# Performance work log

Hardware: AMD Instinct MI355X
Metric: run time of the kernel (lower is better)

Reference implementation:

```python
import jax, jax.numpy as jnp
import numpy as np

N = 100000        # unique nodes in batch (node_num)
IN_DIM = 256
OUT_DIM = 128
E_RAND = 1_600_000  # random graph edges (avg degree 16)
B = N             # batch nodes (all nodes, each gets a self-loop edge)
SLOPE = 0.1       # leaky_relu slope_ratio


def setup_inputs() -> dict:
    key = jax.random.key(0)
    k1, k2, k3, k4, k5, k6 = jax.random.split(key, 6)
    x = jax.random.normal(k1, (N, IN_DIM), dtype=jnp.float32)
    # small weight scale keeps exp(leaky_relu(.)) in a sane range, like kaiming on unit-ish inputs
    W = jax.random.normal(k2, (OUT_DIM, IN_DIM), dtype=jnp.float32) * 0.05
    b = jax.random.normal(k3, (OUT_DIM,), dtype=jnp.float32) * 0.05
    a = jax.random.normal(k4, (2 * OUT_DIM, 1), dtype=jnp.float32) * 0.05
    src = jax.random.randint(k5, (E_RAND,), 0, N, dtype=jnp.int32)
    dst = jax.random.randint(k6, (E_RAND,), 0, N, dtype=jnp.int32)
    batch_idx = jnp.arange(B, dtype=jnp.int32)
    # append self-loop edges for every batch node (original vstacks original_node_edge)
    edges = jnp.stack([jnp.concatenate([src, batch_idx]),
                       jnp.concatenate([dst, batch_idx])], axis=1)  # [E_TOT, 2]
    return {"x": x, "W": W, "b": b, "a": a, "edges": edges, "batch_idx": batch_idx}


def reference(x, W, b, a, edges, batch_idx):
    # new_embeddings = Linear(in_dim -> out_dim)
    emb = x @ W.T + b  # [N, out_dim]
    # concat(h_src, h_dst) @ a  ==  h_src @ a[:d] + h_dst @ a[d:]
    a1 = a[:OUT_DIM, 0]
    a2 = a[OUT_DIM:, 0]
    s_src = emb @ a1  # [N]
    s_dst = emb @ a2  # [N]
    src, dst = edges[:, 0], edges[:, 1]
    logits = s_src[src] + s_dst[dst]                                 # [E]
    score = jnp.exp(jax.nn.leaky_relu(logits, negative_slope=SLOPE))  # [E]
    # sparse row-sum and aggregation fused as segment reductions over src
    row_sum = jax.ops.segment_sum(score, src, num_segments=N)        # [N]
    msgs = score[:, None] * emb[dst]                                 # [E, out_dim]
    results = jax.ops.segment_sum(msgs, src, num_segments=N)         # [N, out_dim]
    # nodes with no outgoing edges have row_sum==0; they are never gathered below
    safe_rs = jnp.where(row_sum > 0, row_sum, 1.0)
    out = results / safe_rs[:, None]
    return out[batch_idx]
```

## Files before the change

kernel.cpp:

```cpp
#include <hip/hip_runtime.h>
#include <hip/hip_fp16.h>

#define IN_DIM 256
#define OUT_DIM 128
#define SLOPE 0.1f

typedef __attribute__((ext_vector_type(8))) short short8;
typedef __attribute__((ext_vector_type(4))) float f32x4;

__device__ __forceinline__ unsigned bf16_rne(float f) {
    unsigned u = __float_as_uint(f);
    return (u + 0x7FFFu + ((u >> 16) & 1u)) >> 16;
}

__global__ __launch_bounds__(256) void wsplit_kernel(
    const float* __restrict__ W, short* __restrict__ Whi, short* __restrict__ Wlo)
{
    const int i = blockIdx.x * 256 + threadIdx.x;
    const float v = W[i];
    const unsigned hb = bf16_rne(v);
    const float hf = __uint_as_float(hb << 16);
    Whi[i] = (short)hb;
    Wlo[i] = (short)bf16_rne(v - hf);
}

__global__ __launch_bounds__(256) void gemm_emb_kernel(
    const float* __restrict__ x, const short* __restrict__ Whi_g,
    const short* __restrict__ Wlo_g, const float* __restrict__ bias,
    const float* __restrict__ a, __half* __restrict__ emb_h,
    float* __restrict__ s1, float* __restrict__ s2, int N)
{
    __shared__ short lds[12288];
    short* Ahi = lds;
    short* Alo = lds + 2048;
    short* Bhi = lds + 4096;
    short* Blo = lds + 8192;

    const int tid = threadIdx.x;
    const int l   = tid & 63;
    const int w   = tid >> 6;
    const int gm0 = blockIdx.x * 64;

    const int arow = tid >> 2;
    const int akc  = tid & 3;
    const int gmA  = gm0 + arow;
    const bool av_ok = (gmA < N);
    const int brow = tid >> 1;
    const int bkc0 = (tid & 1) * 2;

    f32x4 acc[8];
    #pragma unroll
    for (int j = 0; j < 8; ++j) acc[j] = (f32x4)0.f;

    float bias_v[8], av1[8], av2[8];
    #pragma unroll
    for (int nf = 0; nf < 8; ++nf) {
        const int col = nf * 16 + (l & 15);
        bias_v[nf] = bias[col];
        av1[nf]    = a[col];
        av2[nf]    = a[OUT_DIM + col];
    }

    for (int ks = 0; ks < 8; ++ks) {
        const int k0 = ks * 32;
        {
            float v[8];
            if (av_ok) {
                const float4 p0 = *(const float4*)&x[(size_t)gmA * IN_DIM + k0 + akc * 8];
                const float4 p1 = *(const float4*)&x[(size_t)gmA * IN_DIM + k0 + akc * 8 + 4];
                v[0]=p0.x; v[1]=p0.y; v[2]=p0.z; v[3]=p0.w;
                v[4]=p1.x; v[5]=p1.y; v[6]=p1.z; v[7]=p1.w;
            } else {
                #pragma unroll
                for (int j = 0; j < 8; ++j) v[j] = 0.f;
            }
            short8 h8, l8;
            #pragma unroll
            for (int j = 0; j < 8; ++j) {
                unsigned hb = bf16_rne(v[j]);
                float hf = __uint_as_float(hb << 16);
                h8[j] = (short)hb;
                l8[j] = (short)bf16_rne(v[j] - hf);
            }
            *(short8*)&Ahi[akc * 512 + arow * 8] = h8;
            *(short8*)&Alo[akc * 512 + arow * 8] = l8;
        }
        #pragma unroll
        for (int q = 0; q < 2; ++q) {
            const int kc = bkc0 + q;
            const short8 h8 = *(const short8*)&Whi_g[brow * IN_DIM + k0 + kc * 8];
            const short8 l8 = *(const short8*)&Wlo_g[brow * IN_DIM + k0 + kc * 8];
            *(short8*)&Bhi[kc * 1024 + brow * 8] = h8;
            *(short8*)&Blo[kc * 1024 + brow * 8] = l8;
        }
        __syncthreads();

        const int arow_f = w * 16 + (l & 15);
        const int aoff   = (l >> 4) * 512 + arow_f * 8;
        const short8 ah = *(const short8*)&Ahi[aoff];
        const short8 al = *(const short8*)&Alo[aoff];
        #pragma unroll
        for (int nf = 0; nf < 8; ++nf) {
            const int col = nf * 16 + (l & 15);
            const int boff = (l >> 4) * 1024 + col * 8;
            const short8 bh = *(const short8*)&Bhi[boff];
            const short8 bl = *(const short8*)&Blo[boff];
            acc[nf] = __builtin_amdgcn_mfma_f32_16x16x32_bf16(ah, bh, acc[nf], 0, 0, 0);
            acc[nf] = __builtin_amdgcn_mfma_f32_16x16x32_bf16(al, bh, acc[nf], 0, 0, 0);
            acc[nf] = __builtin_amdgcn_mfma_f32_16x16x32_bf16(ah, bl, acc[nf], 0, 0, 0);
        }
        __syncthreads();
    }

    __half* hl = (__half*)lds;
    #pragma unroll
    for (int r = 0; r < 4; ++r) {
        const int lrow = w * 16 + (l >> 4) * 4 + r;
        float p1 = 0.f, p2 = 0.f;
        #pragma unroll
        for (int nf = 0; nf < 8; ++nf) {
            const float e = acc[nf][r] + bias_v[nf];
            p1 += e * av1[nf];
            p2 += e * av2[nf];
            hl[lrow * 144 + nf * 16 + (l & 15)] = __float2half(e);
        }
        p1 += __shfl_xor(p1, 1); p1 += __shfl_xor(p1, 2);
        p1 += __shfl_xor(p1, 4); p1 += __shfl_xor(p1, 8);
        p2 += __shfl_xor(p2, 1); p2 += __shfl_xor(p2, 2);
        p2 += __shfl_xor(p2, 4); p2 += __shfl_xor(p2, 8);
        const int gm = gm0 + lrow;
        if ((l & 15) == 0 && gm < N) { s1[gm] = p1; s2[gm] = p2; }
    }
    __syncthreads();
    #pragma unroll
    for (int i = 0; i < 4; ++i) {
        const int idx = i * 256 + tid;
        const int row = idx >> 4, seg = idx & 15;
        if (gm0 + row < N) {
            const uint4 u = *(const uint4*)&hl[row * 144 + seg * 8];
            ((uint4*)emb_h)[(size_t)(gm0 + row) * 16 + seg] = u;
        }
    }
}

__global__ __launch_bounds__(256) void rank_kernel(
    const int* __restrict__ edges, int* __restrict__ deg,
    int* __restrict__ rank, int E)
{
    const int e0 = (blockIdx.x * 256 + threadIdx.x) * 4;
    if (e0 + 3 < E) {
        const int4 ea = ((const int4*)edges)[(e0 >> 1) + 0];
        const int4 eb = ((const int4*)edges)[(e0 >> 1) + 1];
        const int r0 = atomicAdd(&deg[ea.x], 1);
        const int r1 = atomicAdd(&deg[ea.z], 1);
        const int r2 = atomicAdd(&deg[eb.x], 1);
        const int r3 = atomicAdd(&deg[eb.z], 1);
        ((int4*)rank)[e0 >> 2] = make_int4(r0, r1, r2, r3);
    } else if (e0 < E) {
        for (int e = e0; e < E; ++e) {
            const int2 ed = ((const int2*)edges)[e];
            rank[e] = atomicAdd(&deg[ed.x], 1);
        }
    }
}

__global__ __launch_bounds__(256) void scan1_kernel(
    const int* __restrict__ deg, int* __restrict__ off,
    int* __restrict__ bsum, int N)
{
    __shared__ int lds[256];
    const int t = threadIdx.x;
    const int base = blockIdx.x * 1024 + t * 4;
    int v[4];
    int ts = 0;
    #pragma unroll
    for (int j = 0; j < 4; ++j) {
        v[j] = (base + j < N) ? deg[base + j] : 0;
        ts += v[j];
    }
    lds[t] = ts;
    __syncthreads();
    for (int d = 1; d < 256; d <<= 1) {
        int xv = (t >= d) ? lds[t - d] : 0;
        __syncthreads();
        lds[t] += xv;
        __syncthreads();
    }
    int run = lds[t] - ts;
    #pragma unroll
    for (int j = 0; j < 4; ++j) {
        if (base + j < N) off[base + j] = run;
        run += v[j];
    }
    if (t == 255) bsum[blockIdx.x] = lds[255];
}

__global__ __launch_bounds__(256) void scan2_kernel(int* __restrict__ bsum, int nb)
{
    __shared__ int lds[256];
    const int t = threadIdx.x;
    const int v = (t < nb) ? bsum[t] : 0;
    lds[t] = v;
    __syncthreads();
    for (int d = 1; d < 256; d <<= 1) {
        int xv = (t >= d) ? lds[t - d] : 0;
        __syncthreads();
        lds[t] += xv;
        __syncthreads();
    }
    if (t < nb) bsum[t] = lds[t] - v;
}

__global__ __launch_bounds__(256) void scan3_kernel(
    int* __restrict__ off, const int* __restrict__ bsum,
    const int* __restrict__ bidx, int* __restrict__ flag, int N, int E)
{
    const int i = blockIdx.x * 256 + threadIdx.x;
    if (i < N) {
        off[i] += bsum[i >> 10];
        if (bidx[i] != i) atomicOr(flag, 1);
    }
    if (i == 0) off[N] = E;
}

__global__ __launch_bounds__(256) void fill_kernel(
    const int* __restrict__ edges, const int* __restrict__ off,
    const int* __restrict__ rank, int* __restrict__ csr, int E)
{
    const int e0 = (blockIdx.x * 256 + threadIdx.x) * 4;
    if (e0 + 3 < E) {
        const int4 ea = ((const int4*)edges)[(e0 >> 1) + 0];
        const int4 eb = ((const int4*)edges)[(e0 >> 1) + 1];
        const int4 rk = ((const int4*)rank)[e0 >> 2];
        csr[off[ea.x] + rk.x] = ea.y;
        csr[off[ea.z] + rk.y] = ea.w;
        csr[off[eb.x] + rk.z] = eb.y;
        csr[off[eb.z] + rk.w] = eb.w;
    } else if (e0 < E) {
        for (int e = e0; e < E; ++e) {
            const int2 ed = ((const int2*)edges)[e];
            csr[off[ed.x] + rank[e]] = ed.y;
        }
    }
}

__global__ __launch_bounds__(256) void agg_kernel(
    const int* __restrict__ off, const int* __restrict__ csr,
    const float* __restrict__ s1, const float* __restrict__ s2,
    const __half* __restrict__ emb_h, const int* __restrict__ flag,
    float* __restrict__ results, float* __restrict__ out, int N)
{
    const int wid  = (int)((blockIdx.x * 256u + threadIdx.x) >> 6);
    const int lane = threadIdx.x & 63;
    if (wid >= N) return;
    const int eg = lane >> 4;
    const int cl = lane & 15;
    const int beg = off[wid];
    const int end = off[wid + 1];
    const float s1n = s1[wid];

    const float4* __restrict__ embrow = (const float4*)emb_h;

    float av[8];
    #pragma unroll
    for (int k = 0; k < 8; ++k) av[k] = 0.f;
    float rs = 0.f;

    for (int base = beg; base < end; base += 16) {
        int dq[4];
        #pragma unroll
        for (int q = 0; q < 4; ++q) {
            const int idx = base + q * 4 + eg;
            dq[q] = (idx < end) ? csr[idx] : -1;
        }
        float scq[4];
        #pragma unroll
        for (int q = 0; q < 4; ++q) {
            if (dq[q] >= 0) {
                const float ll = s1n + s2[dq[q]];
                scq[q] = __expf(ll > 0.f ? ll : SLOPE * ll);
            } else {
                scq[q] = 0.f;
                dq[q]  = 0;
            }
        }
        float4 vq[4];
        #pragma unroll
        for (int q = 0; q < 4; ++q)
            vq[q] = embrow[(size_t)dq[q] * 16 + cl];
        #pragma unroll
        for (int q = 0; q < 4; ++q) {
            rs += scq[q];
            const __half2* hp = reinterpret_cast<const __half2*>(&vq[q]);
            #pragma unroll
            for (int k = 0; k < 4; ++k) {
                const float2 f = __half22float2(hp[k]);
                av[2 * k]     += scq[q] * f.x;
                av[2 * k + 1] += scq[q] * f.y;
            }
        }
    }

    #pragma unroll
    for (int k = 0; k < 8; ++k) {
        av[k] += __shfl_xor(av[k], 16);
        av[k] += __shfl_xor(av[k], 32);
    }
    rs += __shfl_xor(rs, 16);
    rs += __shfl_xor(rs, 32);

    const float inv = 1.f / (rs > 0.f ? rs : 1.f);
    if (eg == 0) {
        float* dbuf = (*flag == 0) ? out : results;
        float4* rp = (float4*)&dbuf[(size_t)wid * 128 + cl * 8];
        rp[0] = make_float4(av[0] * inv, av[1] * inv, av[2] * inv, av[3] * inv);
        rp[1] = make_float4(av[4] * inv, av[5] * inv, av[6] * inv, av[7] * inv);
    }
}

__global__ __launch_bounds__(256) void gather_kernel(
    const float* __restrict__ results, const int* __restrict__ bidx,
    const int* __restrict__ flag, float* __restrict__ out, int N)
{
    if (*flag == 0) return;
    const unsigned i = blockIdx.x * 256u + threadIdx.x;
    if (i >= (unsigned)N * 32u) return;
    const unsigned n = i >> 5, c = i & 31;
    ((float4*)out)[i] = ((const float4*)results)[(size_t)bidx[n] * 32 + c];
}

extern "C" void kernel_launch(void* const* d_in, const int* in_sizes, int n_in,
                              void* d_out, int out_size, void* d_ws, size_t ws_size,
                              hipStream_t stream) {
    const float* x     = (const float*)d_in[0];
    const float* W     = (const float*)d_in[1];
    const float* b     = (const float*)d_in[2];
    const float* a     = (const float*)d_in[3];
    const int*   edges = (const int*)d_in[4];
    const int*   bidx  = (const int*)d_in[5];

    const int N = in_sizes[5];
    const int E = in_sizes[4] / 2;

    float*  results = (float*)d_ws;
    __half* emb_h   = (__half*)(results + (size_t)N * OUT_DIM);
    int*    rank    = (int*)(emb_h + (size_t)N * OUT_DIM);
    int*    csr     = rank + E;
    float*  s1      = (float*)(csr + E);
    float*  s2      = s1 + N;
    int*    deg     = (int*)(s2 + N);
    int*    flag    = deg + N;
    int*    off     = flag + 1;
    int*    bsum    = off + N + 1;
    short*  Whi     = (short*)(bsum + 256);
    short*  Wlo     = Whi + OUT_DIM * IN_DIM;

    hipMemsetAsync(deg, 0, (size_t)(N + 1) * sizeof(int), stream);

    wsplit_kernel<<<(OUT_DIM * IN_DIM) / 256, 256, 0, stream>>>(W, Whi, Wlo);

    dim3 gGemm((N + 63) / 64);
    gemm_emb_kernel<<<gGemm, 256, 0, stream>>>(x, Whi, Wlo, b, a, emb_h, s1, s2, N);

    const int gE4 = (E / 4 + 255) / 256 + 1;
    rank_kernel<<<gE4, 256, 0, stream>>>(edges, deg, rank, E);

    const int nb = (N + 1023) / 1024;
    scan1_kernel<<<nb, 256, 0, stream>>>(deg, off, bsum, N);
    scan2_kernel<<<1, 256, 0, stream>>>(bsum, nb);
    scan3_kernel<<<(N + 255) / 256, 256, 0, stream>>>(off, bsum, bidx, flag, N, E);

    fill_kernel<<<gE4, 256, 0, stream>>>(edges, off, rank, csr, E);

    const unsigned aggThreads = (unsigned)N * 64u;
    agg_kernel<<<(aggThreads + 255u) / 256u, 256, 0, stream>>>(
        off, csr, s1, s2, emb_h, flag, results, (float*)d_out, N);

    const unsigned gatherThreads = (unsigned)N * 32u;
    gather_kernel<<<(gatherThreads + 255u) / 256u, 256, 0, stream>>>(
        results, bidx, flag, (float*)d_out, N);
}
```

Before: 229.7 us.

## Stage edge scores in LDS per wave and fold block-sum scan into scan3

The aggregation kernel now computes each edge's destination index and attention score once per lane (64 edges per tile), stashes them in a per-wave LDS slot, and then has the four 16-lane groups read them back to issue up to 8 embedding-row loads at a time. This removes the redundant s2 gathers and exp evaluations that each lane group previously did, and raises memory-level parallelism per iteration. Separately, the single-block scan2 kernel is removed: scan3 now sums the preceding block sums itself with a shared-memory reduction, saving one launch at the cost of redundant small reductions in every block.

```diff
diff --git a/kernel.cpp b/kernel.cpp
--- a/kernel.cpp
+++ b/kernel.cpp
@@ -195,29 +195,26 @@
     if (t == 255) bsum[blockIdx.x] = lds[255];
 }
 
-__global__ __launch_bounds__(256) void scan2_kernel(int* __restrict__ bsum, int nb)
-{
-    __shared__ int lds[256];
-    const int t = threadIdx.x;
-    const int v = (t < nb) ? bsum[t] : 0;
-    lds[t] = v;
-    __syncthreads();
-    for (int d = 1; d < 256; d <<= 1) {
-        int xv = (t >= d) ? lds[t - d] : 0;
-        __syncthreads();
-        lds[t] += xv;
-        __syncthreads();
-    }
-    if (t < nb) bsum[t] = lds[t] - v;
-}
-
 __global__ __launch_bounds__(256) void scan3_kernel(
     int* __restrict__ off, const int* __restrict__ bsum,
     const int* __restrict__ bidx, int* __restrict__ flag, int N, int E)
 {
-    const int i = blockIdx.x * 256 + threadIdx.x;
+    __shared__ int red[256];
+    const int t = threadIdx.x;
+    const int chunk = (int)(blockIdx.x >> 2);
+    int s = 0;
+    for (int j = t; j < chunk; j += 256) s += bsum[j];
+    red[t] = s;
+    __syncthreads();
+    #pragma unroll
+    for (int d = 128; d > 0; d >>= 1) {
+        if (t < d) red[t] += red[t + d];
+        __syncthreads();
+    }
+    const int pref = red[0];
+    const int i = blockIdx.x * 256 + t;
     if (i < N) {
-        off[i] += bsum[i >> 10];
+        off[i] += pref;
         if (bidx[i] != i) atomicOr(flag, 1);
     }
     if (i == 0) off[N] = E;
@@ -250,8 +247,11 @@
     const __half* __restrict__ emb_h, const int* __restrict__ flag,
     float* __restrict__ results, float* __restrict__ out, int N)
 {
+    __shared__ int2 sl[4][64];
+
     const int wid  = (int)((blockIdx.x * 256u + threadIdx.x) >> 6);
     const int lane = threadIdx.x & 63;
+    const int wv   = threadIdx.x >> 6;
     if (wid >= N) return;
     const int eg = lane >> 4;
     const int cl = lane & 15;
@@ -260,54 +260,61 @@
     const float s1n = s1[wid];
 
     const float4* __restrict__ embrow = (const float4*)emb_h;
+    int2* slot = &sl[wv][0];
 
     float av[8];
     #pragma unroll
     for (int k = 0; k < 8; ++k) av[k] = 0.f;
-    float rs = 0.f;
-
-    for (int base = beg; base < end; base += 16) {
-        int dq[4];
-        #pragma unroll
-        for (int q = 0; q < 4; ++q) {
-            const int idx = base + q * 4 + eg;
-            dq[q] = (idx < end) ? csr[idx] : -1;
-        }
-        float scq[4];
-        #pragma unroll
-        for (int q = 0; q < 4; ++q) {
-            if (dq[q] >= 0) {
-                const float ll = s1n + s2[dq[q]];
-                scq[q] = __expf(ll > 0.f ? ll : SLOPE * ll);
-            } else {
-                scq[q] = 0.f;
-                dq[q]  = 0;
+    float rsl = 0.f;
+
+    for (int tile = beg; tile < end; tile += 64) {
+        const int cnt = min(64, end - tile);
+        int d = 0; float sc = 0.f;
+        if (lane < cnt) {
+            d = csr[tile + lane];
+            const float ll = s1n + s2[d];
+            sc = __expf(ll > 0.f ? ll : SLOPE * ll);
+        }
+        rsl += sc;
+        slot[lane] = make_int2(d, __float_as_int(sc));
+        __builtin_amdgcn_wave_barrier();
+        for (int j0 = 0; j0 < cnt; j0 += 32) {
+            const int nq = ((cnt - j0) + 3) >> 2;
+            int dq[8]; float scq[8];
+            #pragma unroll
+            for (int q = 0; q < 8; ++q) {
+                dq[q] = 0; scq[q] = 0.f;
+                if (q < nq) {
+                    const int2 p = slot[j0 + q * 4 + eg];
+                    dq[q] = p.x; scq[q] = __int_as_float(p.y);
+                }
             }
-        }
-        float4 vq[4];
-        #pragma unroll
-        for (int q = 0; q < 4; ++q)
-            vq[q] = embrow[(size_t)dq[q] * 16 + cl];
-        #pragma unroll
-        for (int q = 0; q < 4; ++q) {
-            rs += scq[q];
-            const __half2* hp = reinterpret_cast<const __half2*>(&vq[q]);
+            float4 vq[8];
             #pragma unroll
-            for (int k = 0; k < 4; ++k) {
-                const float2 f = __half22float2(hp[k]);
-                av[2 * k]     += scq[q] * f.x;
-                av[2 * k + 1] += scq[q] * f.y;
+            for (int q = 0; q < 8; ++q)
+                if (q < nq) vq[q] = embrow[(size_t)dq[q] * 16 + cl];
+            #pragma unroll
+            for (int q = 0; q < 8; ++q) {
+                if (q < nq) {
+                    const __half* hp = reinterpret_cast<const __half*>(&vq[q]);
+                    #pragma unroll
+                    for (int k = 0; k < 8; ++k)
+                        av[k] += scq[q] * __half2float(hp[k]);
+                }
             }
         }
-    }
-
+        __builtin_amdgcn_wave_barrier();
+    }
+
+    float rs = rsl;
+    rs += __shfl_xor(rs, 1);  rs += __shfl_xor(rs, 2);
+    rs += __shfl_xor(rs, 4);  rs += __shfl_xor(rs, 8);
+    rs += __shfl_xor(rs, 16); rs += __shfl_xor(rs, 32);
     #pragma unroll
     for (int k = 0; k < 8; ++k) {
         av[k] += __shfl_xor(av[k], 16);
         av[k] += __shfl_xor(av[k], 32);
     }
-    rs += __shfl_xor(rs, 16);
-    rs += __shfl_xor(rs, 32);
 
     const float inv = 1.f / (rs > 0.f ? rs : 1.f);
     if (eg == 0) {
@@ -367,7 +374,6 @@
 
     const int nb = (N + 1023) / 1024;
     scan1_kernel<<<nb, 256, 0, stream>>>(deg, off, bsum, N);
-    scan2_kernel<<<1, 256, 0, stream>>>(bsum, nb);
     scan3_kernel<<<(N + 255) / 256, 256, 0, stream>>>(off, bsum, bidx, flag, N, E);
 
     fill_kernel<<<gE4, 256, 0, stream>>>(edges, off, rank, csr, E);
```

Measured after the change: 225.1 us. 1.02x faster.
